# Performance work log

Measured on AMD Instinct MI355X. Metric: run time of the kernel, lower is better.

## Reference

```python
import jax, jax.numpy as jnp
import numpy as np

NUM_SUPERPIXELS = 256


def setup_inputs() -> dict:
    key = jax.random.key(0)
    k1, k2 = jax.random.split(key)
    B, H, W, C = 8, 512, 512, 64
    feature_map = jax.random.normal(k1, (B, H, W, C), dtype=jnp.float32)
    superpixel_map = jax.random.randint(k2, (B, H, W), 0, NUM_SUPERPIXELS, dtype=jnp.int32)
    return {"feature_map": feature_map, "superpixel_map": superpixel_map}


def reference(feature_map, superpixel_map):
    # feature_map: [B,H,W,C] float; superpixel_map: [B,H,W] int labels in [0, S)
    B, H, W, C = feature_map.shape
    S = NUM_SUPERPIXELS
    num_segments = B * S
    feat = feature_map.reshape(-1, C)                       # [B*H*W, C]
    batch_ids = jnp.arange(B, dtype=jnp.int32)[:, None, None]
    seg = (batch_ids * S + superpixel_map).reshape(-1)      # global segment id [B*H*W]
    sums = jax.ops.segment_sum(feat, seg, num_segments=num_segments)          # [B*S, C]
    counts = jax.ops.segment_sum(jnp.ones((seg.shape[0],), feat.dtype), seg,
                                 num_segments=num_segments)                    # [B*S]
    means = sums / jnp.maximum(counts, 1.0)[:, None]        # empty segments -> 0
    return means.reshape(B, S, C)
```

## Files before the change

kernel.cpp:

```cpp
#include <hip/hip_runtime.h>


#define NBATCH 8
#define NSEG 256
#define NCH 64
#define PPB (512 * 512)
#define BPB 64
#define PIX_PER_BLOCK 4096
#define NWAVE 8
#define NCHUNK 16
#define CHUNK_PIX 256
#define QMAX 264
#define NROWS (NSEG + NWAVE)

__global__ __launch_bounds__(512, 2) void pool_kernel(const float* __restrict__ feat,
                                                      const int* __restrict__ sp,
                                                      float* __restrict__ pspart,
                                                      unsigned* __restrict__ pscnt) {
    __shared__ float hist[NROWS * NCH];
    __shared__ unsigned cnt[NROWS];
    __shared__ int qd[NWAVE][QMAX];

    const int b = blockIdx.x >> 6;
    const int slab = blockIdx.x & 63;
    const int tid = threadIdx.x;
    const int lane = tid & 63;
    const int wave = tid >> 6;

    for (int i = tid; i < (NROWS * NCH) / 4; i += 512)
        ((float4*)hist)[i] = make_float4(0.f, 0.f, 0.f, 0.f);
    if (tid < NROWS) cnt[tid] = 0u;
    __syncthreads();

    const int pixbase = slab * PIX_PER_BLOCK;
    const int4* lp4 = (const int4*)(sp + (size_t)b * PPB + pixbase);
    const float* fb = feat + ((size_t)b * PPB + pixbase) * NCH + lane;

    const int dummy_e = (NSEG + wave) << 12;
    int* q = qd[wave];

    int4 lab = lp4[lane];
    for (int c = 0; c < NCHUNK; ++c) {
        const int cn = (c + 1 < NCHUNK) ? (c + 1) : c;
        int4 nlab = lp4[cn * 64 + lane];
        int qn = 0;
        const int pbase = c * CHUNK_PIX + 4 * lane;

#define PUSH(SV, CC)                                                          \
        {                                                                     \
            const int s_ = (SV);                                              \
            const bool own_ = ((s_ >> 5) == wave);                            \
            const unsigned long long m_ = __ballot(own_);                     \
            if (own_) {                                                       \
                const int r_ = __builtin_amdgcn_mbcnt_hi(                     \
                    (unsigned)(m_ >> 32),                                     \
                    __builtin_amdgcn_mbcnt_lo((unsigned)m_, 0));              \
                q[qn + r_] = (s_ << 12) | (pbase + (CC));                     \
                atomicAdd(&cnt[s_], 1u);                                      \
            }                                                                 \
            qn += __builtin_popcountll(m_);                                   \
        }
        PUSH(lab.x, 0) PUSH(lab.y, 1) PUSH(lab.z, 2) PUSH(lab.w, 3)
#undef PUSH

        const int npad = (8 - (qn & 7)) & 7;
        if (lane < npad) q[qn + lane] = dummy_e;
        qn += npad;

        const int ng = qn >> 3;
        if (ng) {
            int4 a0 = *(const int4*)&q[0];
            int4 a1 = *(const int4*)&q[4];
            float f0 = fb[(size_t)(a0.x & 4095) * NCH];
            float f1 = fb[(size_t)(a0.y & 4095) * NCH];
            float f2 = fb[(size_t)(a0.z & 4095) * NCH];
            float f3 = fb[(size_t)(a0.w & 4095) * NCH];
            float f4 = fb[(size_t)(a1.x & 4095) * NCH];
            float f5 = fb[(size_t)(a1.y & 4095) * NCH];
            float f6 = fb[(size_t)(a1.z & 4095) * NCH];
            float f7 = fb[(size_t)(a1.w & 4095) * NCH];
            for (int g = 1; g < ng; ++g) {
                int4 b0 = *(const int4*)&q[g * 8];
                int4 b1 = *(const int4*)&q[g * 8 + 4];
                float h0 = fb[(size_t)(b0.x & 4095) * NCH];
                float h1 = fb[(size_t)(b0.y & 4095) * NCH];
                float h2 = fb[(size_t)(b0.z & 4095) * NCH];
                float h3 = fb[(size_t)(b0.w & 4095) * NCH];
                float h4 = fb[(size_t)(b1.x & 4095) * NCH];
                float h5 = fb[(size_t)(b1.y & 4095) * NCH];
                float h6 = fb[(size_t)(b1.z & 4095) * NCH];
                float h7 = fb[(size_t)(b1.w & 4095) * NCH];

                hist[(a0.x >> 12) * NCH + lane] += f0;
                hist[(a0.y >> 12) * NCH + lane] += f1;
                hist[(a0.z >> 12) * NCH + lane] += f2;
                hist[(a0.w >> 12) * NCH + lane] += f3;
                hist[(a1.x >> 12) * NCH + lane] += f4;
                hist[(a1.y >> 12) * NCH + lane] += f5;
                hist[(a1.z >> 12) * NCH + lane] += f6;
                hist[(a1.w >> 12) * NCH + lane] += f7;

                a0 = b0; a1 = b1;
                f0 = h0; f1 = h1; f2 = h2; f3 = h3;
                f4 = h4; f5 = h5; f6 = h6; f7 = h7;
            }
            hist[(a0.x >> 12) * NCH + lane] += f0;
            hist[(a0.y >> 12) * NCH + lane] += f1;
            hist[(a0.z >> 12) * NCH + lane] += f2;
            hist[(a0.w >> 12) * NCH + lane] += f3;
            hist[(a1.x >> 12) * NCH + lane] += f4;
            hist[(a1.y >> 12) * NCH + lane] += f5;
            hist[(a1.z >> 12) * NCH + lane] += f6;
            hist[(a1.w >> 12) * NCH + lane] += f7;
        }
        lab = nlab;
    }
    __syncthreads();

    float4* wp = (float4*)(pspart + (size_t)blockIdx.x * (NSEG * NCH));
    const float4* hs = (const float4*)hist;
    for (int i = tid; i < (NSEG * NCH) / 4; i += 512) wp[i] = hs[i];
    if (tid < NSEG) pscnt[(size_t)blockIdx.x * NSEG + tid] = cnt[tid];
}

__global__ __launch_bounds__(64) void reduce_kernel(const float* __restrict__ pspart,
                                                    const unsigned* __restrict__ pscnt,
                                                    float* __restrict__ out) {
    const int bs = blockIdx.x;
    const int bnum = bs >> 8;
    const int seg = bs & 255;
    const int lane = threadIdx.x;

    const float* base = pspart + ((size_t)bnum * BPB * NSEG + seg) * NCH + lane;
    float acc = 0.f;
#pragma unroll
    for (int s = 0; s < BPB; ++s)
        acc += base[(size_t)s * NSEG * NCH];

    unsigned c = pscnt[((size_t)bnum * BPB + lane) * NSEG + seg];
    for (int o = 32; o; o >>= 1) c += __shfl_xor(c, o);

    out[(size_t)bs * NCH + lane] = acc / (float)(c > 0u ? c : 1u);
}

extern "C" void kernel_launch(void* const* d_in, const int* in_sizes, int n_in,
                              void* d_out, int out_size, void* d_ws, size_t ws_size,
                              hipStream_t stream) {
    const float* feat = (const float*)d_in[0];
    const int* sp = (const int*)d_in[1];
    float* out = (float*)d_out;
    float* pspart = (float*)d_ws;
    unsigned* pscnt = (unsigned*)((char*)d_ws + (size_t)NBATCH * BPB * NSEG * NCH * 4);
    (void)in_sizes; (void)n_in; (void)out_size; (void)ws_size;

    pool_kernel<<<NBATCH * BPB, 512, 0, stream>>>(feat, sp, pspart, pscnt);
    reduce_kernel<<<NBATCH * NSEG, 64, 0, stream>>>(pspart, pscnt, out);
}
```

Measured before the change: 694.2 us.

## Stage feature tiles through shared memory with register double-buffering

Each block now loads contiguous 128-pixel feature tiles into LDS with coalesced float4 loads, prefetching the next tile into registers while the current one is processed. Waves then gather pixel features from LDS instead of issuing scattered per-pixel global loads. This replaces uncoalesced global gathers with streaming loads. In exchange it adds two block barriers per round, uses 32 KB more LDS, which may lower occupancy, and processes smaller queues in 4-element groups.

```diff
diff --git a/kernel.cpp b/kernel.cpp
--- a/kernel.cpp
+++ b/kernel.cpp
@@ -8,9 +8,10 @@
 #define BPB 64
 #define PIX_PER_BLOCK 4096
 #define NWAVE 8
-#define NCHUNK 16
-#define CHUNK_PIX 256
-#define QMAX 264
+#define TILE_PX 128
+#define ROUNDS (PIX_PER_BLOCK / TILE_PX)
+#define PXW (TILE_PX / NWAVE)
+#define QMAX 132
 #define NROWS (NSEG + NWAVE)
 
 __global__ __launch_bounds__(512, 2) void pool_kernel(const float* __restrict__ feat,
@@ -18,8 +19,9 @@
                                                       float* __restrict__ pspart,
                                                       unsigned* __restrict__ pscnt) {
     __shared__ float hist[NROWS * NCH];
+    __shared__ float tile[TILE_PX * NCH];
+    __shared__ int qd[NWAVE][QMAX];
     __shared__ unsigned cnt[NROWS];
-    __shared__ int qd[NWAVE][QMAX];
 
     const int b = blockIdx.x >> 6;
     const int slab = blockIdx.x & 63;
@@ -30,23 +32,34 @@
     for (int i = tid; i < (NROWS * NCH) / 4; i += 512)
         ((float4*)hist)[i] = make_float4(0.f, 0.f, 0.f, 0.f);
     if (tid < NROWS) cnt[tid] = 0u;
-    __syncthreads();
 
-    const int pixbase = slab * PIX_PER_BLOCK;
-    const int4* lp4 = (const int4*)(sp + (size_t)b * PPB + pixbase);
-    const float* fb = feat + ((size_t)b * PPB + pixbase) * NCH + lane;
+    const int gpix0 = slab * PIX_PER_BLOCK;
+    const float4* fbase = (const float4*)(feat + ((size_t)b * PPB + gpix0) * NCH);
+    const int2* lp2 = (const int2*)(sp + (size_t)b * PPB + gpix0);
 
-    const int dummy_e = (NSEG + wave) << 12;
+    const int dummy_e = (NSEG + wave) << 8;
     int* q = qd[wave];
+    float4* t4 = (float4*)tile;
+    const int wslice = wave * PXW * 16;
 
-    int4 lab = lp4[lane];
-    for (int c = 0; c < NCHUNK; ++c) {
-        const int cn = (c + 1 < NCHUNK) ? (c + 1) : c;
-        int4 nlab = lp4[cn * 64 + lane];
+    float4 buf0, buf1, buf2, buf3;
+#define STAGE_LOAD(R)                                                         \
+    {   const int fb_ = ((R) * TILE_PX) * 16 + wslice;                        \
+        buf0 = fbase[fb_ + lane];        buf1 = fbase[fb_ + 64 + lane];       \
+        buf2 = fbase[fb_ + 128 + lane];  buf3 = fbase[fb_ + 192 + lane];  }
+#define STAGE_WRITE()                                                         \
+    {   t4[wslice + lane] = buf0;        t4[wslice + 64 + lane] = buf1;       \
+        t4[wslice + 128 + lane] = buf2;  t4[wslice + 192 + lane] = buf3;  }
+
+    STAGE_LOAD(0);
+    STAGE_WRITE();
+    for (int r = 0; r < ROUNDS; ++r) {
+        if (r + 1 < ROUNDS) STAGE_LOAD(r + 1);
+        __syncthreads();
+
+        const int2 L = lp2[r * 64 + lane];
         int qn = 0;
-        const int pbase = c * CHUNK_PIX + 4 * lane;
-
-#define PUSH(SV, CC)                                                          \
+#define PUSH(SV, PX)                                                          \
         {                                                                     \
             const int s_ = (SV);                                              \
             const bool own_ = ((s_ >> 5) == wave);                            \
@@ -55,65 +68,33 @@
                 const int r_ = __builtin_amdgcn_mbcnt_hi(                     \
                     (unsigned)(m_ >> 32),                                     \
                     __builtin_amdgcn_mbcnt_lo((unsigned)m_, 0));              \
-                q[qn + r_] = (s_ << 12) | (pbase + (CC));                     \
+                q[qn + r_] = (s_ << 8) | (PX);                                \
                 atomicAdd(&cnt[s_], 1u);                                      \
             }                                                                 \
             qn += __builtin_popcountll(m_);                                   \
         }
-        PUSH(lab.x, 0) PUSH(lab.y, 1) PUSH(lab.z, 2) PUSH(lab.w, 3)
+        PUSH(L.x, 2 * lane)
+        PUSH(L.y, 2 * lane + 1)
 #undef PUSH
-
-        const int npad = (8 - (qn & 7)) & 7;
+        const int npad = (4 - (qn & 3)) & 3;
         if (lane < npad) q[qn + lane] = dummy_e;
         qn += npad;
 
-        const int ng = qn >> 3;
-        if (ng) {
-            int4 a0 = *(const int4*)&q[0];
-            int4 a1 = *(const int4*)&q[4];
-            float f0 = fb[(size_t)(a0.x & 4095) * NCH];
-            float f1 = fb[(size_t)(a0.y & 4095) * NCH];
-            float f2 = fb[(size_t)(a0.z & 4095) * NCH];
-            float f3 = fb[(size_t)(a0.w & 4095) * NCH];
-            float f4 = fb[(size_t)(a1.x & 4095) * NCH];
-            float f5 = fb[(size_t)(a1.y & 4095) * NCH];
-            float f6 = fb[(size_t)(a1.z & 4095) * NCH];
-            float f7 = fb[(size_t)(a1.w & 4095) * NCH];
-            for (int g = 1; g < ng; ++g) {
-                int4 b0 = *(const int4*)&q[g * 8];
-                int4 b1 = *(const int4*)&q[g * 8 + 4];
-                float h0 = fb[(size_t)(b0.x & 4095) * NCH];
-                float h1 = fb[(size_t)(b0.y & 4095) * NCH];
-                float h2 = fb[(size_t)(b0.z & 4095) * NCH];
-                float h3 = fb[(size_t)(b0.w & 4095) * NCH];
-                float h4 = fb[(size_t)(b1.x & 4095) * NCH];
-                float h5 = fb[(size_t)(b1.y & 4095) * NCH];
-                float h6 = fb[(size_t)(b1.z & 4095) * NCH];
-                float h7 = fb[(size_t)(b1.w & 4095) * NCH];
+        const int ng = qn >> 2;
+        for (int g = 0; g < ng; ++g) {
+            const int4 e = *(const int4*)&q[g * 4];
+            const float v0 = tile[(e.x & 255) * NCH + lane];
+            const float v1 = tile[(e.y & 255) * NCH + lane];
+            const float v2 = tile[(e.z & 255) * NCH + lane];
+            const float v3 = tile[(e.w & 255) * NCH + lane];
+            hist[(e.x >> 8) * NCH + lane] += v0;
+            hist[(e.y >> 8) * NCH + lane] += v1;
+            hist[(e.z >> 8) * NCH + lane] += v2;
+            hist[(e.w >> 8) * NCH + lane] += v3;
+        }
 
-                hist[(a0.x >> 12) * NCH + lane] += f0;
-                hist[(a0.y >> 12) * NCH + lane] += f1;
-                hist[(a0.z >> 12) * NCH + lane] += f2;
-                hist[(a0.w >> 12) * NCH + lane] += f3;
-                hist[(a1.x >> 12) * NCH + lane] += f4;
-                hist[(a1.y >> 12) * NCH + lane] += f5;
-                hist[(a1.z >> 12) * NCH + lane] += f6;
-                hist[(a1.w >> 12) * NCH + lane] += f7;
-
-                a0 = b0; a1 = b1;
-                f0 = h0; f1 = h1; f2 = h2; f3 = h3;
-                f4 = h4; f5 = h5; f6 = h6; f7 = h7;
-            }
-            hist[(a0.x >> 12) * NCH + lane] += f0;
-            hist[(a0.y >> 12) * NCH + lane] += f1;
-            hist[(a0.z >> 12) * NCH + lane] += f2;
-            hist[(a0.w >> 12) * NCH + lane] += f3;
-            hist[(a1.x >> 12) * NCH + lane] += f4;
-            hist[(a1.y >> 12) * NCH + lane] += f5;
-            hist[(a1.z >> 12) * NCH + lane] += f6;
-            hist[(a1.w >> 12) * NCH + lane] += f7;
-        }
-        lab = nlab;
+        __syncthreads();
+        if (r + 1 < ROUNDS) STAGE_WRITE();
     }
     __syncthreads();
 
```

Result: slower. 725.4 us (+4.5%).
